# Optimization experiments

Measured on AMD Instinct MI355X. Metric: run time of the kernel, lower is better.

Reference implementation:

```python
import jax, jax.numpy as jnp
import numpy as np

E = 128
H = 4
D = E // H  # 32


def setup_inputs() -> dict:
    key = jax.random.key(0)
    ks = jax.random.split(key, 5)
    b, n = 4, 4096
    x = jax.random.normal(ks[0], (b, n, E), dtype=jnp.float32)
    # Linear weights stored as [in, out] (i.e. torch weight transposed)
    W_qkv = jax.random.normal(ks[1], (E, 3 * E), dtype=jnp.float32) * (1.0 / np.sqrt(E))
    b_qkv = jax.random.normal(ks[2], (3 * E,), dtype=jnp.float32) * 0.01
    W_proj = jax.random.normal(ks[3], (E, E), dtype=jnp.float32) * (1.0 / np.sqrt(E))
    b_proj = jax.random.normal(ks[4], (E,), dtype=jnp.float32) * 0.01
    return {"x": x, "W_qkv": W_qkv, "b_qkv": b_qkv, "W_proj": W_proj, "b_proj": b_proj}


def reference(x, W_qkv, b_qkv, W_proj, b_proj):
    b, n, e = x.shape
    # qkv projection; last dim layout is (h d qkv) with qkv innermost,
    # matching rearrange('b n (h d qkv) -> qkv b h n d')
    qkv = (x @ W_qkv + b_qkv).reshape(b, n, H, D, 3)
    qkv = jnp.transpose(qkv, (4, 0, 2, 1, 3))  # [3, b, h, n, d]
    q, k, v = qkv[0], qkv[1], qkv[2]
    # NOTE: original scales by sqrt(e) (=sqrt(128)), not sqrt(d). Faithful.
    scale = 1.0 / np.float32(np.sqrt(e))
    scores = jnp.einsum('bhnd,bhmd->bhnm', q, k) * scale  # [b,h,n,n]
    att = jax.nn.softmax(scores, axis=-1)
    # dropout is identity in eval mode (reference baseline)
    out = jnp.einsum('bhnm,bhmd->bhnd', att, v)  # [b,h,n,d]
    out = jnp.transpose(out, (0, 2, 1, 3)).reshape(b, n, e)  # b n (h d)
    return out @ W_proj + b_proj
```

## Files before the change

kernel.cpp:

```cpp
#include <hip/hip_runtime.h>
#include <stdint.h>

#define N_SEQ 4096
#define MFMA16 __builtin_amdgcn_mfma_f32_16x16x32_bf16

typedef float f32x4 __attribute__((ext_vector_type(4)));
typedef float f32x2 __attribute__((ext_vector_type(2)));
typedef unsigned short u16x8 __attribute__((ext_vector_type(8)));
typedef unsigned short u16x4 __attribute__((ext_vector_type(4)));
typedef unsigned int u32x2 __attribute__((ext_vector_type(2)));
typedef __bf16 bf16x8 __attribute__((ext_vector_type(8)));

static __device__ __forceinline__ float bf2f(unsigned short u) {
    unsigned v = ((unsigned)u) << 16;
    return __builtin_bit_cast(float, v);
}

__global__ __launch_bounds__(256) void wrepack_kernel(
    const float* __restrict__ Wq, unsigned short* __restrict__ WqF)
{
    int idx = blockIdx.x * 256 + threadIdx.x;
    int i = idx & 7, l = (idx >> 3) & 63, fr = idx >> 9;
    int ct = fr >> 2, ks = fr & 3;
    int k = ks * 32 + (l >> 4) * 8 + i;
    int col = ct * 16 + (l & 15);
    WqF[idx] = __builtin_bit_cast(unsigned short, (__bf16)Wq[k * 384 + col]);
}

__global__ __launch_bounds__(256) void qkv_kernel(
    const float* __restrict__ x, const unsigned short* __restrict__ WqF,
    const float* __restrict__ bq, unsigned short* __restrict__ Qo,
    unsigned short* __restrict__ KFo, unsigned short* __restrict__ VFo)
{
    const int tid = threadIdx.x, lane = tid & 63, w = tid >> 6;
    const int g = lane >> 4, lo = lane & 15;
    const long r0 = (long)blockIdx.x * 32;
    const float SL = (float)(0.08838834764831845 * 1.4426950408889634);
    const f32x4 zf = {0.f, 0.f, 0.f, 0.f};

    bf16x8 xf[2][4];
    #pragma unroll
    for (int rt = 0; rt < 2; ++rt) {
        const float* xr = x + (r0 + rt * 16 + lo) * 128 + g * 8;
        #pragma unroll
        for (int ks = 0; ks < 4; ++ks) {
            f32x4 a = *(const f32x4*)&xr[ks * 32];
            f32x4 b = *(const f32x4*)&xr[ks * 32 + 4];
            bf16x8 f;
            f[0] = (__bf16)a[0]; f[1] = (__bf16)a[1]; f[2] = (__bf16)a[2]; f[3] = (__bf16)a[3];
            f[4] = (__bf16)b[0]; f[5] = (__bf16)b[1]; f[6] = (__bf16)b[2]; f[7] = (__bf16)b[3];
            xf[rt][ks] = f;
        }
    }
    f32x4 acc[2][6];
    #pragma unroll
    for (int rt = 0; rt < 2; ++rt)
        #pragma unroll
        for (int c = 0; c < 6; ++c) acc[rt][c] = zf;

    const u16x8* wp = (const u16x8*)WqF + (size_t)(w * 24) * 64 + lane;
    #pragma unroll
    for (int c = 0; c < 6; ++c)
        #pragma unroll
        for (int ks = 0; ks < 4; ++ks) {
            bf16x8 wf = __builtin_bit_cast(bf16x8, wp[(c * 4 + ks) * 64]);
            acc[0][c] = MFMA16(xf[0][ks], wf, acc[0][c], 0, 0, 0);
            acc[1][c] = MFMA16(xf[1][ks], wf, acc[1][c], 0, 0, 0);
        }

    const int bb = (int)(r0 >> 12), nn0 = (int)(r0 & 4095);
    const int bh = bb * 4 + w;
    const int t = nn0 >> 6, kvb = nn0 & 63;
    const int kk = kvb >> 5;
    #pragma unroll
    for (int c = 0; c < 6; ++c) {
        int col = (w * 6 + c) * 16 + lo;
        int rem = col - w * 96;
        int d = rem / 3, s = rem % 3;
        float bias = bq[col];
        #pragma unroll
        for (int rt = 0; rt < 2; ++rt) {
            float scale = (s == 0) ? SL : 1.0f;
            unsigned short bits[4];
            #pragma unroll
            for (int j = 0; j < 4; ++j)
                bits[j] = __builtin_bit_cast(unsigned short,
                              (__bf16)((acc[rt][c][j] + bias) * scale));
            if (s == 0) {
                long base = ((long)bh * 4096 + nn0 + rt * 16 + 4 * g) * 32 + d;
                #pragma unroll
                for (int j = 0; j < 4; ++j) Qo[base + (long)j * 32] = bits[j];
            } else if (s == 1) {
                int ct_k = (kvb >> 4) + rt;
                long base = (long)((bh * 64 + t) * 4 + ct_k) * 512
                          + ((d >> 3) * 16 + 4 * g) * 8 + (d & 7);
                #pragma unroll
                for (int j = 0; j < 4; ++j) KFo[base + j * 8] = bits[j];
            } else {
                int lg = rt * 2 + (g >> 1);
                long base = (long)(((bh * 64 + t) * 2 + kk) * 2 + (d >> 4)) * 512
                          + (lg * 16 + (d & 15)) * 8 + ((4 * g) & 7);
                u16x4 pk = {bits[0], bits[1], bits[2], bits[3]};
                *(u16x4*)&VFo[base] = pk;
            }
        }
    }
}

__global__ __launch_bounds__(256, 4) void attn_kernel(
    const unsigned short* __restrict__ Q, const unsigned short* __restrict__ KF,
    const unsigned short* __restrict__ VF, unsigned short* __restrict__ AO)
{
    __shared__ __align__(16) unsigned char smem[19456];

    const int tid = threadIdx.x, lane = tid & 63, w = tid >> 6;
    const int g = lane >> 4, lo = lane & 15;

    const int bid = blockIdx.x;
    const int vid = (bid & 7) * 256 + (bid >> 3);
    const int qi = vid & 127, bh = vid >> 7;
    const int q0 = qi * 32;

    bf16x8 qf[2];
    #pragma unroll
    for (int rt = 0; rt < 2; ++rt) {
        const unsigned short* p = Q + ((long)bh * 4096 + q0 + rt * 16 + lo) * 32 + g * 8;
        qf[rt] = __builtin_bit_cast(bf16x8, *(const u16x8*)p);
    }
    bf16x8 onesf;
    {
        u16x8 ou = {0x3F80,0x3F80,0x3F80,0x3F80,0x3F80,0x3F80,0x3F80,0x3F80};
        onesf = __builtin_bit_cast(bf16x8, ou);
    }
    const f32x4 zf = {0.f, 0.f, 0.f, 0.f};
    f32x4 o_[2][2] = {{zf, zf}, {zf, zf}};
    f32x4 ls[2]    = {zf, zf};

    int woff[2][4], roff[2][2];
    #pragma unroll
    for (int qt = 0; qt < 2; ++qt) {
        int q = lo + 16 * qt;
        #pragma unroll
        for (int ct = 0; ct < 4; ++ct) {
            int kvb = 16 * ct + 4 * g;
            woff[qt][ct] = q * 64 + (((kvb >> 3) ^ (q & 7)) * 8) + ((kvb >> 2) & 1) * 4;
        }
    }
    #pragma unroll
    for (int rt = 0; rt < 2; ++rt) {
        int q = lo + 16 * rt;
        #pragma unroll
        for (int kk = 0; kk < 2; ++kk)
            roff[rt][kk] = q * 64 + ((((4 * kk) + g) ^ (q & 7)) * 8);
    }
    unsigned short* B = (unsigned short*)(smem + w * 4096);

    const u16x8* kp = (const u16x8*)KF + ((long)bh * 64 + w * 16) * 256 + lane;
    const u16x8* vp = (const u16x8*)VF + ((long)bh * 64 + w * 16) * 256 + lane;

    u16x8 K0[4], K1[4], V0[4], V1[4];
    #pragma unroll
    for (int i = 0; i < 4; ++i) K0[i] = kp[i * 64];
    kp += 256;

#define BODY(KC, KN, VP, VC, DOPV) do {                                        \
    _Pragma("unroll")                                                          \
    for (int i = 0; i < 4; ++i) KN[i] = kp[i * 64];                            \
    kp += 256;                                                                 \
    _Pragma("unroll")                                                          \
    for (int i = 0; i < 4; ++i) VC[i] = vp[i * 64];                            \
    vp += 256;                                                                 \
    u16x8 pa_[2][2];                                                           \
    if (DOPV) {                                                                \
        _Pragma("unroll")                                                      \
        for (int kk = 0; kk < 2; ++kk)                                         \
            _Pragma("unroll")                                                  \
            for (int rt = 0; rt < 2; ++rt)                                     \
                pa_[kk][rt] = *(const u16x8*)&B[roff[rt][kk]];                 \
    }                                                                          \
    f32x4 s_[2][4];                                                            \
    _Pragma("unroll")                                                          \
    for (int ct = 0; ct < 4; ++ct) {                                           \
        bf16x8 kfr = __builtin_bit_cast(bf16x8, KC[ct]);                       \
        s_[0][ct] = MFMA16(kfr, qf[0], zf, 0, 0, 0);                           \
        s_[1][ct] = MFMA16(kfr, qf[1], zf, 0, 0, 0);                           \
    }                                                                          \
    if (DOPV) {                                                                \
        _Pragma("unroll")                                                      \
        for (int kk = 0; kk < 2; ++kk)                                         \
            _Pragma("unroll")                                                  \
            for (int rt = 0; rt < 2; ++rt) {                                   \
                bf16x8 paf = __builtin_bit_cast(bf16x8, pa_[kk][rt]);          \
                ls[rt] = MFMA16(paf, onesf, ls[rt], 0, 0, 0);                  \
                o_[rt][0] = MFMA16(paf, __builtin_bit_cast(bf16x8, VP[kk*2+0]),\
                                   o_[rt][0], 0, 0, 0);                        \
                o_[rt][1] = MFMA16(paf, __builtin_bit_cast(bf16x8, VP[kk*2+1]),\
                                   o_[rt][1], 0, 0, 0);                        \
            }                                                                  \
    }                                                                          \
    _Pragma("unroll")                                                          \
    for (int qt = 0; qt < 2; ++qt)                                             \
        _Pragma("unroll")                                                      \
        for (int ct = 0; ct < 4; ++ct) {                                       \
            unsigned b0 = __builtin_bit_cast(unsigned,                         \
                __builtin_amdgcn_exp2f(s_[qt][ct][0])) + 0x8000u;              \
            unsigned b1 = __builtin_bit_cast(unsigned,                         \
                __builtin_amdgcn_exp2f(s_[qt][ct][1])) + 0x8000u;              \
            unsigned b2 = __builtin_bit_cast(unsigned,                         \
                __builtin_amdgcn_exp2f(s_[qt][ct][2])) + 0x8000u;              \
            unsigned b3 = __builtin_bit_cast(unsigned,                         \
                __builtin_amdgcn_exp2f(s_[qt][ct][3])) + 0x8000u;              \
            u32x2 wv_;                                                         \
            wv_[0] = __builtin_amdgcn_perm(b1, b0, 0x07060302u);               \
            wv_[1] = __builtin_amdgcn_perm(b3, b2, 0x07060302u);               \
            *(u16x4*)&B[woff[qt][ct]] = __builtin_bit_cast(u16x4, wv_);        \
        }                                                                      \
    __builtin_amdgcn_sched_barrier(0);                                         \
} while (0)

    BODY(K0, K1, V1, V0, 0);
    #pragma unroll 1
    for (int t = 1; t < 15; t += 2) {
        BODY(K1, K0, V0, V1, 1);
        BODY(K0, K1, V1, V0, 1);
    }
    BODY(K1, K0, V0, V1, 1);
#undef BODY

    #pragma unroll
    for (int kk = 0; kk < 2; ++kk)
        #pragma unroll
        for (int rt = 0; rt < 2; ++rt) {
            bf16x8 paf = __builtin_bit_cast(bf16x8, *(const u16x8*)&B[roff[rt][kk]]);
            ls[rt] = MFMA16(paf, onesf, ls[rt], 0, 0, 0);
            o_[rt][0] = MFMA16(paf, __builtin_bit_cast(bf16x8, V1[kk*2+0]), o_[rt][0], 0, 0, 0);
            o_[rt][1] = MFMA16(paf, __builtin_bit_cast(bf16x8, V1[kk*2+1]), o_[rt][1], 0, 0, 0);
        }

    __syncthreads();
    float* comb = (float*)smem;
    if (w > 0) {
        float* myp = comb + ((w - 1) * 64 + lane) * 25;
        #pragma unroll
        for (int rt = 0; rt < 2; ++rt)
            #pragma unroll
            for (int dt = 0; dt < 2; ++dt)
                *(f32x4*)&myp[(rt * 2 + dt) * 4] = o_[rt][dt];
        *(f32x4*)&myp[16] = ls[0];
        *(f32x4*)&myp[20] = ls[1];
    }
    __syncthreads();
    if (w == 0) {
        #pragma unroll
        for (int i = 0; i < 3; ++i) {
            const float* pp = comb + (i * 64 + lane) * 25;
            #pragma unroll
            for (int rt = 0; rt < 2; ++rt) {
                #pragma unroll
                for (int dt = 0; dt < 2; ++dt)
                    o_[rt][dt] += *(const f32x4*)&pp[(rt * 2 + dt) * 4];
                ls[rt] += *(const f32x4*)&pp[16 + rt * 4];
            }
        }
        const int bb = bh >> 2, h = bh & 3;
        #pragma unroll
        for (int rt = 0; rt < 2; ++rt)
            #pragma unroll
            for (int j = 0; j < 4; ++j) {
                float rl = __builtin_amdgcn_rcpf(ls[rt][j]);
                int row = q0 + rt * 16 + 4 * g + j;
                #pragma unroll
                for (int dt = 0; dt < 2; ++dt) {
                    int e = h * 32 + lo + 16 * dt;
                    float val = o_[rt][dt][j] * rl;
                    AO[((long)bb * N_SEQ + row) * 128 + e] =
                        __builtin_bit_cast(unsigned short, (__bf16)val);
                }
            }
    }
}

__global__ __launch_bounds__(256) void proj_kernel(
    const unsigned short* __restrict__ ain, const float* __restrict__ Wp,
    const float* __restrict__ bp, float* __restrict__ out)
{
    __shared__ __align__(16) float xT[128][36];
    const int tid = threadIdx.x;
    const long r0 = (long)blockIdx.x * 32;
    #pragma unroll
    for (int i = 0; i < 2; ++i) {
        int idx = i * 256 + tid;
        int row = idx >> 4, kc = (idx & 15) * 8;
        u16x8 v = *(const u16x8*)&ain[(r0 + row) * 128 + kc];
        #pragma unroll
        for (int e = 0; e < 8; ++e) xT[kc + e][row] = bf2f(v[e]);
    }
    __syncthreads();
    const int r8 = (tid >> 6) * 8;
    const int c  = tid & 63;
    float acc0[8], acc1[8];
    #pragma unroll
    for (int r = 0; r < 8; ++r) { acc0[r] = 0.f; acc1[r] = 0.f; }
    for (int k = 0; k < 128; ++k) {
        f32x4 a0 = *(const f32x4*)&xT[k][r8];
        f32x4 a1 = *(const f32x4*)&xT[k][r8 + 4];
        float xr[8] = {a0[0],a0[1],a0[2],a0[3],a1[0],a1[1],a1[2],a1[3]};
        float w0 = Wp[k * 128 + c];
        float w1 = Wp[k * 128 + c + 64];
        #pragma unroll
        for (int r = 0; r < 8; ++r) {
            acc0[r] = fmaf(xr[r], w0, acc0[r]);
            acc1[r] = fmaf(xr[r], w1, acc1[r]);
        }
    }
    float b0 = bp[c], b1 = bp[c + 64];
    #pragma unroll
    for (int r = 0; r < 8; ++r) {
        long n = r0 + r8 + r;
        out[n * 128 + c]      = acc0[r] + b0;
        out[n * 128 + c + 64] = acc1[r] + b1;
    }
}

extern "C" void kernel_launch(void* const* d_in, const int* in_sizes, int n_in,
                              void* d_out, int out_size, void* d_ws, size_t ws_size,
                              hipStream_t stream)
{
    const float* x  = (const float*)d_in[0];
    const float* Wq = (const float*)d_in[1];
    const float* bq = (const float*)d_in[2];
    const float* Wp = (const float*)d_in[3];
    const float* bp = (const float*)d_in[4];
    float* out = (float*)d_out;

    unsigned short* Qw   = (unsigned short*)d_ws;
    unsigned short* KFw  = Qw  + (size_t)16 * 4096 * 32;
    unsigned short* VFw  = KFw + (size_t)16 * 4096 * 32;
    unsigned short* AOw  = VFw + (size_t)16 * 4096 * 32;
    unsigned short* WqFw = AOw + (size_t)16 * 4096 * 32;

    wrepack_kernel<<<192, 256, 0, stream>>>(Wq, WqFw);
    qkv_kernel<<<512, 256, 0, stream>>>(x, WqFw, bq, Qw, KFw, VFw);
    attn_kernel<<<2048, 256, 0, stream>>>(Qw, KFw, VFw, AOw);
    proj_kernel<<<512, 256, 0, stream>>>(AOw, Wp, bp, out);
}
```

Baseline: 95.70 us.

## Use bf16 MFMA for output projection, raise attention occupancy, truncate P rounding

```diff
diff --git a/kernel.cpp b/kernel.cpp
--- a/kernel.cpp
+++ b/kernel.cpp
@@ -25,6 +25,17 @@
     int k = ks * 32 + (l >> 4) * 8 + i;
     int col = ct * 16 + (l & 15);
     WqF[idx] = __builtin_bit_cast(unsigned short, (__bf16)Wq[k * 384 + col]);
+}
+
+__global__ __launch_bounds__(256) void wrepack2_kernel(
+    const float* __restrict__ Wp, unsigned short* __restrict__ WpF)
+{
+    int idx = blockIdx.x * 256 + threadIdx.x;
+    int i = idx & 7, l = (idx >> 3) & 63, fr = idx >> 9;
+    int ct = fr >> 2, ks = fr & 3;
+    int k = ks * 32 + (l >> 4) * 8 + i;
+    int col = ct * 16 + (l & 15);
+    WpF[idx] = __builtin_bit_cast(unsigned short, (__bf16)Wp[k * 128 + col]);
 }
 
 __global__ __launch_bounds__(256) void qkv_kernel(
@@ -107,7 +118,7 @@
     }
 }
 
-__global__ __launch_bounds__(256, 4) void attn_kernel(
+__global__ __launch_bounds__(256, 8) void attn_kernel(
     const unsigned short* __restrict__ Q, const unsigned short* __restrict__ KF,
     const unsigned short* __restrict__ VF, unsigned short* __restrict__ AO)
 {
@@ -203,13 +214,13 @@
         _Pragma("unroll")                                                      \
         for (int ct = 0; ct < 4; ++ct) {                                       \
             unsigned b0 = __builtin_bit_cast(unsigned,                         \
-                __builtin_amdgcn_exp2f(s_[qt][ct][0])) + 0x8000u;              \
+                __builtin_amdgcn_exp2f(s_[qt][ct][0]));                        \
             unsigned b1 = __builtin_bit_cast(unsigned,                         \
-                __builtin_amdgcn_exp2f(s_[qt][ct][1])) + 0x8000u;              \
+                __builtin_amdgcn_exp2f(s_[qt][ct][1]));                        \
             unsigned b2 = __builtin_bit_cast(unsigned,                         \
-                __builtin_amdgcn_exp2f(s_[qt][ct][2])) + 0x8000u;              \
+                __builtin_amdgcn_exp2f(s_[qt][ct][2]));                        \
             unsigned b3 = __builtin_bit_cast(unsigned,                         \
-                __builtin_amdgcn_exp2f(s_[qt][ct][3])) + 0x8000u;              \
+                __builtin_amdgcn_exp2f(s_[qt][ct][3]));                        \
             u32x2 wv_;                                                         \
             wv_[0] = __builtin_amdgcn_perm(b1, b0, 0x07060302u);               \
             wv_[1] = __builtin_amdgcn_perm(b3, b2, 0x07060302u);               \
@@ -281,44 +292,45 @@
 }
 
 __global__ __launch_bounds__(256) void proj_kernel(
-    const unsigned short* __restrict__ ain, const float* __restrict__ Wp,
+    const unsigned short* __restrict__ AO, const unsigned short* __restrict__ WpF,
     const float* __restrict__ bp, float* __restrict__ out)
 {
-    __shared__ __align__(16) float xT[128][36];
-    const int tid = threadIdx.x;
+    const int tid = threadIdx.x, lane = tid & 63, w = tid >> 6;
+    const int g = lane >> 4, lo = lane & 15;
     const long r0 = (long)blockIdx.x * 32;
-    #pragma unroll
-    for (int i = 0; i < 2; ++i) {
-        int idx = i * 256 + tid;
-        int row = idx >> 4, kc = (idx & 15) * 8;
-        u16x8 v = *(const u16x8*)&ain[(r0 + row) * 128 + kc];
-        #pragma unroll
-        for (int e = 0; e < 8; ++e) xT[kc + e][row] = bf2f(v[e]);
-    }
-    __syncthreads();
-    const int r8 = (tid >> 6) * 8;
-    const int c  = tid & 63;
-    float acc0[8], acc1[8];
-    #pragma unroll
-    for (int r = 0; r < 8; ++r) { acc0[r] = 0.f; acc1[r] = 0.f; }
-    for (int k = 0; k < 128; ++k) {
-        f32x4 a0 = *(const f32x4*)&xT[k][r8];
-        f32x4 a1 = *(const f32x4*)&xT[k][r8 + 4];
-        float xr[8] = {a0[0],a0[1],a0[2],a0[3],a1[0],a1[1],a1[2],a1[3]};
-        float w0 = Wp[k * 128 + c];
-        float w1 = Wp[k * 128 + c + 64];
-        #pragma unroll
-        for (int r = 0; r < 8; ++r) {
-            acc0[r] = fmaf(xr[r], w0, acc0[r]);
-            acc1[r] = fmaf(xr[r], w1, acc1[r]);
-        }
-    }
-    float b0 = bp[c], b1 = bp[c + 64];
-    #pragma unroll
-    for (int r = 0; r < 8; ++r) {
-        long n = r0 + r8 + r;
-        out[n * 128 + c]      = acc0[r] + b0;
-        out[n * 128 + c + 64] = acc1[r] + b1;
+    const f32x4 zf = {0.f, 0.f, 0.f, 0.f};
+
+    bf16x8 xf[2][4];
+    #pragma unroll
+    for (int rt = 0; rt < 2; ++rt) {
+        const unsigned short* xr = AO + (r0 + rt * 16 + lo) * 128 + g * 8;
+        #pragma unroll
+        for (int ks = 0; ks < 4; ++ks)
+            xf[rt][ks] = __builtin_bit_cast(bf16x8, *(const u16x8*)&xr[ks * 32]);
+    }
+    f32x4 acc[2][2] = {{zf, zf}, {zf, zf}};
+
+    const u16x8* wp = (const u16x8*)WpF + (size_t)(w * 8) * 64 + lane;
+    #pragma unroll
+    for (int c = 0; c < 2; ++c)
+        #pragma unroll
+        for (int ks = 0; ks < 4; ++ks) {
+            bf16x8 wf = __builtin_bit_cast(bf16x8, wp[(c * 4 + ks) * 64]);
+            acc[0][c] = MFMA16(xf[0][ks], wf, acc[0][c], 0, 0, 0);
+            acc[1][c] = MFMA16(xf[1][ks], wf, acc[1][c], 0, 0, 0);
+        }
+
+    #pragma unroll
+    for (int c = 0; c < 2; ++c) {
+        int col = (w * 2 + c) * 16 + lo;
+        float bias = bp[col];
+        #pragma unroll
+        for (int rt = 0; rt < 2; ++rt) {
+            long base = (r0 + rt * 16 + 4 * g) * 128 + col;
+            #pragma unroll
+            for (int j = 0; j < 4; ++j)
+                out[base + (long)j * 128] = acc[rt][c][j] + bias;
+        }
     }
 }
 
@@ -334,13 +346,15 @@
     float* out = (float*)d_out;
 
     unsigned short* Qw   = (unsigned short*)d_ws;
-    unsigned short* KFw  = Qw  + (size_t)16 * 4096 * 32;
-    unsigned short* VFw  = KFw + (size_t)16 * 4096 * 32;
-    unsigned short* AOw  = VFw + (size_t)16 * 4096 * 32;
-    unsigned short* WqFw = AOw + (size_t)16 * 4096 * 32;
+    unsigned short* KFw  = Qw   + (size_t)16 * 4096 * 32;
+    unsigned short* VFw  = KFw  + (size_t)16 * 4096 * 32;
+    unsigned short* AOw  = VFw  + (size_t)16 * 4096 * 32;
+    unsigned short* WqFw = AOw  + (size_t)16 * 4096 * 32;
+    unsigned short* WpFw = WqFw + (size_t)49152;
 
     wrepack_kernel<<<192, 256, 0, stream>>>(Wq, WqFw);
+    wrepack2_kernel<<<64, 256, 0, stream>>>(Wp, WpFw);
     qkv_kernel<<<512, 256, 0, stream>>>(x, WqFw, bq, Qw, KFw, VFw);
     attn_kernel<<<2048, 256, 0, stream>>>(Qw, KFw, VFw, AOw);
-    proj_kernel<<<512, 256, 0, stream>>>(AOw, Wp, bp, out);
-}
+    proj_kernel<<<512, 256, 0, stream>>>(AOw, WpFw, bp, out);
+}
```

New measurement: 281.6 us. +194.3%, slower.
